# Performance work log

Hardware: AMD Instinct MI355X
Metric: run time of the kernel (lower is better)

## Reference

```python
import jax, jax.numpy as jnp
import numpy as np

B, N, E, F, H, OUT = 128, 2048, 16384, 32, 64, 16


def setup_inputs() -> dict:
    key = jax.random.key(0)
    ks = jax.random.split(key, 8)
    node_features = jax.random.normal(ks[0], (B, N, F), jnp.float32)
    edge_index = jax.random.randint(ks[1], (B, 2, E), 0, N)
    n_nodes = jax.random.randint(ks[2], (B,), N // 2, N + 1)
    # prefix node mask (required for the original's index-consistency)
    node_mask = jnp.arange(N)[None, :] < n_nodes[:, None]
    glorot = lambda k, sh, fan: jax.random.normal(k, sh, jnp.float32) / np.sqrt(fan)
    return dict(
        node_features=node_features, edge_index=edge_index, node_mask=node_mask,
        W1=glorot(ks[3], (F, H), F), b1=jnp.zeros((H,), jnp.float32),
        W2=glorot(ks[4], (H, H), H), b2=jnp.zeros((H,), jnp.float32),
        aW1=glorot(ks[5], (H, H), H), ab1=jnp.zeros((H,), jnp.float32),
        aW2=glorot(ks[6], (H, OUT), H), ab2=jnp.zeros((OUT,), jnp.float32),
    )


def reference(node_features, edge_index, node_mask, W1, b1, W2, b2, aW1, ab1, aW2, ab2):
    x = node_features
    src, dst = edge_index[:, 0], edge_index[:, 1]          # [B,E] source->target
    n = node_mask.sum(-1)                                   # [B] valid nodes per graph
    max_idx = n - 1
    emask = (src <= max_idx[:, None]) & (dst <= max_idx[:, None])
    w = emask.astype(x.dtype)                               # [B,E] edge weights

    # flatten batch into one big segment space [B*N]
    offs = (jnp.arange(B, dtype=src.dtype) * N)[:, None]
    src_f = (src + offs).reshape(-1)
    dst_f = (dst + offs).reshape(-1)
    w_f = w.reshape(-1)

    # GCN normalization with self-loops (PyG GCNConv default)
    deg = jax.ops.segment_sum(w_f, dst_f, num_segments=B * N).reshape(B, N)
    deg = deg + node_mask.astype(x.dtype)                   # self-loop weight 1 on valid nodes
    dis = jnp.where(deg > 0, jax.lax.rsqrt(deg), 0.0)       # deg^{-1/2}, [B,N]
    dis_f = dis.reshape(-1)
    norm = dis_f[src_f] * dis_f[dst_f] * w_f                # [B*E]
    nmask_f = node_mask.reshape(-1).astype(x.dtype)[:, None]
    nmask = node_mask.astype(x.dtype)[..., None]

    def gcn_relu(h, W, bias):
        hW = (h @ W).reshape(B * N, -1)                     # transform first (PyG order)
        msgs = hW[src_f] * norm[:, None]                    # [B*E, H]
        agg = jax.ops.segment_sum(msgs, dst_f, num_segments=B * N)
        agg = agg + hW * ((dis * dis).reshape(-1)[:, None] * nmask_f)  # self-loop term
        out = (agg.reshape(B, N, -1) + bias) * nmask
        return jax.nn.relu(out)

    h1 = gcn_relu(x * nmask, W1, b1)
    h2 = gcn_relu(h1, W2, b2)

    # mean pool over valid nodes (zeros if empty graph)
    pooled = h2.sum(1) / jnp.maximum(n, 1)[:, None].astype(x.dtype)
    hidden = jax.nn.relu(pooled @ aW1 + ab1)
    logits = hidden @ aW2 + ab2                             # [B, OUT]
    return logits
```

## Files before the change

### kernel.cpp

```cpp
#include <hip/hip_runtime.h>
#include <hip/hip_bf16.h>

#define B 128
#define N 2048
#define E 16384
#define F 32
#define H 64
#define OUTD 16
#define CAP 16
#define NP1 (N + 1)

typedef __attribute__((ext_vector_type(8))) short bf16x8;
typedef __attribute__((ext_vector_type(4))) float f32x4;

__device__ __forceinline__ float b2f(unsigned short u) {
    return __uint_as_float(((unsigned int)u) << 16);
}
__device__ __forceinline__ unsigned short f2b(float f) {
    unsigned int x = __float_as_uint(f);
    unsigned int r = (x + 0x7FFFu + ((x >> 16) & 1u)) >> 16;
    return (unsigned short)r;
}
__device__ __forceinline__ unsigned int pack2(float a, float b) {
    return (unsigned int)f2b(a) | ((unsigned int)f2b(b) << 16);
}

__device__ __forceinline__ void add8(float (&a)[8], uint4 u) {
    a[0] += __uint_as_float(u.x << 16);
    a[1] += __uint_as_float(u.x & 0xffff0000u);
    a[2] += __uint_as_float(u.y << 16);
    a[3] += __uint_as_float(u.y & 0xffff0000u);
    a[4] += __uint_as_float(u.z << 16);
    a[5] += __uint_as_float(u.z & 0xffff0000u);
    a[6] += __uint_as_float(u.w << 16);
    a[7] += __uint_as_float(u.w & 0xffff0000u);
}
__device__ __forceinline__ void fma8(float (&a)[8], uint4 u, float w) {
    a[0] = fmaf(__uint_as_float(u.x << 16), w, a[0]);
    a[1] = fmaf(__uint_as_float(u.x & 0xffff0000u), w, a[1]);
    a[2] = fmaf(__uint_as_float(u.y << 16), w, a[2]);
    a[3] = fmaf(__uint_as_float(u.y & 0xffff0000u), w, a[3]);
    a[4] = fmaf(__uint_as_float(u.z << 16), w, a[4]);
    a[5] = fmaf(__uint_as_float(u.z & 0xffff0000u), w, a[5]);
    a[6] = fmaf(__uint_as_float(u.w << 16), w, a[6]);
    a[7] = fmaf(__uint_as_float(u.w & 0xffff0000u), w, a[7]);
}

struct PrepArgs {
    const void* src[9];
    void* dst[9];
};

__global__ __launch_bounds__(1024) void k_build(
    const void* __restrict__ x, const int* __restrict__ eidx,
    const void* __restrict__ mask, PrepArgs pa, int* __restrict__ flags,
    int* __restrict__ n_arr, float* __restrict__ dis,
    unsigned char* __restrict__ degc, unsigned short* __restrict__ ssrc,
    int2* __restrict__ ovf, int* __restrict__ ovf_cnt,
    float* __restrict__ pooled, unsigned int* __restrict__ xconv,
    unsigned int* __restrict__ z_u) {
    __shared__ int s_cnt[N];
    __shared__ float s_fred[16];
    __shared__ int s_w[16];
    __shared__ int s_n, s_ovf, s_xbf, s_pf;
    const int b = blockIdx.x;
    const int t = threadIdx.x;
    const int bN = b * N;
    {
        const unsigned short* p = (const unsigned short*)x;
        float s = fminf(fabsf(b2f(p[t])), 1e6f);
        for (int o = 32; o > 0; o >>= 1) s += __shfl_down(s, o);
        if ((t & 63) == 0) s_fred[t >> 6] = s;
        __syncthreads();
        if (t == 0) {
            float a = 0.f;
            for (int i = 0; i < 16; i++) a += s_fred[i];
            int f = (a < 100.0f * 1024.0f) ? 1 : 0;
            s_xbf = f;
            if (b == 0) flags[0] = f;
        }
    }
    const unsigned char* mb = (const unsigned char*)mask;
    int mode;
    if (mb[0] == 0x80 && mb[1] == 0x3F) mode = 2;
    else if (mb[0] != 0 && mb[1] != 0) mode = 0;
    else if (mb[0] != 0) mode = (mb[4] != 0) ? 1 : 4;
    else mode = 3;
    int cnt = 0;
    if (mode == 0) {
        const unsigned char* r = mb + (size_t)b * N;
        for (int i = t; i < N; i += 1024) cnt += (r[i] != 0);
    } else if (mode == 1 || mode == 3) {
        const unsigned int* r = (const unsigned int*)mask + (size_t)b * N;
        for (int i = t; i < N; i += 1024) cnt += (r[i] != 0);
    } else if (mode == 2) {
        const unsigned short* r = (const unsigned short*)mask + (size_t)b * N;
        for (int i = t; i < N; i += 1024) cnt += (r[i] != 0);
    } else {
        const unsigned long long* r = (const unsigned long long*)mask + (size_t)b * N;
        for (int i = t; i < N; i += 1024) cnt += (r[i] != 0ULL);
    }
    for (int o = 32; o > 0; o >>= 1) cnt += __shfl_down(cnt, o);
    if ((t & 63) == 0) s_w[t >> 6] = cnt;
    for (int i = t; i < N; i += 1024) s_cnt[i] = 0;
    if (t >= 32 && t < 64) z_u[((size_t)b * NP1 + N) * (H / 2) + (t - 32)] = 0u;
    if (t == 0) s_ovf = 0;
    __syncthreads();
    if (t == 0) {
        int a = 0;
        for (int i = 0; i < 16; i++) a += s_w[i];
        s_n = a > N ? N : a;
    }
    __syncthreads();
    const int n = s_n;
    const int4* es4 = (const int4*)(eidx + (size_t)b * 2 * E);
    const int4* ed4 = es4 + E / 4;
    int4 sv[4], dv4[4];
#pragma unroll
    for (int k = 0; k < 4; k++) {
        sv[k] = es4[t + k * 1024];
        dv4[k] = ed4[t + k * 1024];
    }
#pragma unroll
    for (int k = 0; k < 4; k++) {
        int4 s4 = sv[k], d4 = dv4[k];
#define FILL1(SS, DD)                                                          \
        if ((unsigned)(SS) < (unsigned)n && (unsigned)(DD) < (unsigned)n) {    \
            int pos = atomicAdd(&s_cnt[DD], 1);                                \
            if (pos < CAP)                                                     \
                ssrc[((size_t)(bN + (DD))) * CAP + pos] = (unsigned short)(SS);\
            else {                                                             \
                int oi = atomicAdd(&s_ovf, 1);                                 \
                if (oi < E) ovf[(size_t)b * E + oi] = make_int2((DD), (SS));   \
            }                                                                  \
        }
        FILL1(s4.x, d4.x) FILL1(s4.y, d4.y) FILL1(s4.z, d4.z) FILL1(s4.w, d4.w)
#undef FILL1
    }
    __syncthreads();
    for (int v = t; v < N; v += 1024) {
        int c = s_cnt[v];
        dis[bN + v] = (v < n) ? rsqrtf((float)(c + 1)) : 0.0f;
        degc[bN + v] = (unsigned char)(c < CAP ? c : CAP);
    }
    if (t < H) pooled[b * H + t] = 0.0f;
    if (t == 0) { n_arr[b] = n; ovf_cnt[b] = s_ovf; }
    if (!s_xbf) {
        const float4* xp = (const float4*)((const float*)x + (size_t)bN * F);
        uint2* yp = (uint2*)(xconv + (size_t)bN * (F / 2));
        for (int i = t; i < N * F / 4; i += 1024) {
            float4 v4 = xp[i];
            yp[i] = make_uint2(pack2(v4.x, v4.y), pack2(v4.z, v4.w));
        }
    }
    if (b >= 1 && b <= 8) {
        int sz;
        switch (b) {
            case 1: sz = F * H; break;
            case 2: sz = H; break;
            case 3: sz = H * H; break;
            case 4: sz = H; break;
            case 5: sz = H * H; break;
            case 6: sz = H; break;
            case 7: sz = H * OUTD; break;
            default: sz = OUTD; break;
        }
        const int K = sz < 1024 ? sz : 1024;
        const unsigned short* p = (const unsigned short*)pa.src[b];
        float s = (t < K) ? fminf(fabsf(b2f(p[t])), 1e6f) : 0.f;
        for (int o = 32; o > 0; o >>= 1) s += __shfl_down(s, o);
        __syncthreads();
        if ((t & 63) == 0) s_fred[t >> 6] = s;
        __syncthreads();
        if (t == 0) {
            float a = 0.f;
            for (int i = 0; i < 16; i++) a += s_fred[i];
            s_pf = (a < 100.0f * (float)K) ? 1 : 0;
        }
        __syncthreads();
        const int fl = s_pf;
        auto rd = [&](int i) -> float {
            return fl ? b2f(((const unsigned short*)pa.src[b])[i])
                      : ((const float*)pa.src[b])[i];
        };
        if (b == 1) {
            unsigned short* dst = (unsigned short*)pa.dst[b];
            for (int i = t; i < F * H; i += 1024) {
                int k = i >> 6, n2 = i & 63;
                dst[n2 * 40 + k] = f2b(rd(i));
            }
        } else if (b == 3) {
            unsigned short* dst = (unsigned short*)pa.dst[b];
            for (int i = t; i < H * H; i += 1024) {
                int k = i >> 6, n2 = i & 63;
                dst[n2 * 72 + k] = f2b(rd(i));
            }
        } else {
            float* dst = (float*)pa.dst[b];
            for (int i = t; i < sz; i += 1024) dst[i] = rd(i);
        }
    }
}

__global__ __launch_bounds__(256) void k_agg_gemm1(
    const void* __restrict__ x, const unsigned int* __restrict__ xconv,
    const int* __restrict__ flags, const float* __restrict__ dis,
    const unsigned char* __restrict__ degc, const unsigned short* __restrict__ ssrc,
    const int2* __restrict__ ovf, const int* __restrict__ ovf_cnt,
    const unsigned short* __restrict__ w1t, const float* __restrict__ b1f,
    unsigned short* __restrict__ zs) {
    __shared__ unsigned short s_e[64 * CAP];
    __shared__ unsigned char s_dg[64];
    __shared__ float s_dv[64];
    __shared__ float s_b1[64];
    __shared__ __align__(16) unsigned short s_w1t[64 * 40];
    __shared__ __align__(16) unsigned short s_a1[64 * 40];
    const int bid = blockIdx.x;
    const int b = (bid & 7) + ((bid >> 8) << 3);
    const int v0 = ((bid >> 3) & 31) * 64;
    const int t = threadIdx.x;
    const int bN = b * N;
    if (t < 128) ((int4*)s_e)[t] = ((const int4*)(ssrc + (size_t)(bN + v0) * CAP))[t];
    if (t >= 128 && t < 144)
        ((unsigned int*)s_dg)[t - 128] = ((const unsigned int*)(degc + bN + v0))[t - 128];
    if (t >= 192) s_dv[t - 192] = dis[bN + v0 + (t - 192)];
    if (t >= 144 && t < 208) s_b1[t - 144] = b1f[t - 144];
    for (int i = t; i < 320; i += 256) ((int4*)s_w1t)[i] = ((const int4*)w1t)[i];
    __syncthreads();
    const int lane = t & 63;
    const int w = t >> 6;
    const int oc = ovf_cnt[b];
    const unsigned int* yb =
        (flags[0] ? (const unsigned int*)x : xconv) + (size_t)bN * (F / 2);
    const float* disb = dis + bN;
    {
        const int nn = w * 16 + (lane >> 2);
        const int v = v0 + nn;
        const int cu = (lane & 3) * 4;
        const int dg = s_dg[nn];
        const float dv = s_dv[nn];
        int md = s_dg[w * 16 + (lane & 15)];
        int m2;
        m2 = __shfl_xor(md, 1); md = md > m2 ? md : m2;
        m2 = __shfl_xor(md, 2); md = md > m2 ? md : m2;
        m2 = __shfl_xor(md, 4); md = md > m2 ? md : m2;
        m2 = __shfl_xor(md, 8); md = md > m2 ? md : m2;
        const unsigned short* ep = &s_e[nn * CAP];
        float a[8] = {0.f, 0.f, 0.f, 0.f, 0.f, 0.f, 0.f, 0.f};
        uint4 rs = *(const uint4*)(yb + (size_t)v * (F / 2) + cu);
        int i0 = ep[0] & (N - 1);
        int i1 = ep[1] & (N - 1);
        uint4 r0 = *(const uint4*)(yb + (size_t)i0 * (F / 2) + cu);
        float w0p = disb[i0];
        uint4 r1 = *(const uint4*)(yb + (size_t)i1 * (F / 2) + cu);
        float w1p = disb[i1];
        fma8(a, rs, dv);
        for (int s = 0; s < md; s++) {
            int sn = s + 2; sn = sn > CAP - 1 ? CAP - 1 : sn;
            int i2 = ep[sn] & (N - 1);
            uint4 r2 = *(const uint4*)(yb + (size_t)i2 * (F / 2) + cu);
            float w2p = disb[i2];
            fma8(a, r0, s < dg ? w0p : 0.0f);
            r0 = r1; w0p = w1p; r1 = r2; w1p = w2p;
        }
        if (oc > 0) {
            const int2* ob = ovf + (size_t)b * E;
            for (int j = 0; j < oc; j++) {
                int2 o = ob[j];
                if (o.x == v) {
                    uint4 u4 = *(const uint4*)(yb + (size_t)o.y * (F / 2) + cu);
                    fma8(a, u4, disb[o.y]);
                }
            }
        }
        uint4 ovv;
        ovv.x = pack2(a[0] * dv, a[1] * dv);
        ovv.y = pack2(a[2] * dv, a[3] * dv);
        ovv.z = pack2(a[4] * dv, a[5] * dv);
        ovv.w = pack2(a[6] * dv, a[7] * dv);
        *(uint4*)((unsigned int*)s_a1 + nn * 20 + cu) = ovv;
    }
    __syncthreads();
    const int quad = lane >> 4;
    const int f2 = lane & 15;
    const int m0 = w * 16;
    bf16x8 af = *(const bf16x8*)&s_a1[(m0 + f2) * 40 + quad * 8];
    float dvr[4];
#pragma unroll
    for (int r = 0; r < 4; r++) dvr[r] = s_dv[m0 + quad * 4 + r];
#pragma unroll
    for (int nt = 0; nt < 4; nt++) {
        bf16x8 bf = *(const bf16x8*)&s_w1t[(nt * 16 + f2) * 40 + quad * 8];
        f32x4 acc = {0.f, 0.f, 0.f, 0.f};
        acc = __builtin_amdgcn_mfma_f32_16x16x32_bf16(af, bf, acc, 0, 0, 0);
        float bb = s_b1[nt * 16 + f2];
#pragma unroll
        for (int r = 0; r < 4; r++) {
            int row = m0 + quad * 4 + r;
            float val = dvr[r] * fmaxf(acc[r] + bb, 0.0f);
            zs[((size_t)b * NP1 + v0 + row) * H + nt * 16 + f2] = f2b(val);
        }
    }
}

__global__ __launch_bounds__(256) void k_agg_gemm2_pool(
    const unsigned int* __restrict__ z_u, const float* __restrict__ dis,
    const unsigned char* __restrict__ degc, const unsigned short* __restrict__ ssrc,
    const int2* __restrict__ ovf, const int* __restrict__ ovf_cnt,
    const unsigned short* __restrict__ w2t, const float* __restrict__ b2f_,
    float* __restrict__ pooled) {
    __shared__ unsigned short s_e[64 * CAP];
    __shared__ unsigned char s_dg[64];
    __shared__ float s_dv[64];
    __shared__ float s_b2[64];
    __shared__ __align__(16) unsigned short s_w2t[64 * 72];
    __shared__ __align__(16) unsigned short s_a2[64 * 72];
    __shared__ float s_pool[4][64];
    const int bid = blockIdx.x;
    const int b = (bid & 7) + ((bid >> 8) << 3);
    const int v0 = ((bid >> 3) & 31) * 64;
    const int t = threadIdx.x;
    const int bN = b * N;
    if (t < 128) ((int4*)s_e)[t] = ((const int4*)(ssrc + (size_t)(bN + v0) * CAP))[t];
    if (t >= 128 && t < 144)
        ((unsigned int*)s_dg)[t - 128] = ((const unsigned int*)(degc + bN + v0))[t - 128];
    if (t >= 192) s_dv[t - 192] = dis[bN + v0 + (t - 192)];
    if (t >= 144 && t < 208) s_b2[t - 144] = b2f_[t - 144];
    for (int i = t; i < 576; i += 256) ((int4*)s_w2t)[i] = ((const int4*)w2t)[i];
    __syncthreads();
    const int lane = t & 63;
    const int w = t >> 6;
    const int oc = ovf_cnt[b];
    const unsigned int* zb = z_u + (size_t)b * NP1 * (H / 2);
#pragma unroll
    for (int g = 0; g < 2; g++) {
        const int nn = w * 16 + g * 8 + (lane >> 3);
        const int v = v0 + nn;
        const int cu = (lane & 7) * 4;
        const int dg = s_dg[nn];
        int md = s_dg[w * 16 + g * 8 + (lane & 7)];
        int m2;
        m2 = __shfl_xor(md, 1); md = md > m2 ? md : m2;
        m2 = __shfl_xor(md, 2); md = md > m2 ? md : m2;
        m2 = __shfl_xor(md, 4); md = md > m2 ? md : m2;
        const unsigned short* ep = &s_e[nn * CAP];
        float a[8] = {0.f, 0.f, 0.f, 0.f, 0.f, 0.f, 0.f, 0.f};
        uint4 cur = *(const uint4*)(zb + (size_t)v * (H / 2) + cu);
        int i0 = (0 < dg) ? (ep[0] & (N - 1)) : N;
        uint4 nxt = *(const uint4*)(zb + (size_t)i0 * (H / 2) + cu);
        for (int s = 0; s < md; s++) {
            int sn = s + 1; sn = sn > CAP - 1 ? CAP - 1 : sn;
            int i2 = (s + 1 < dg) ? (ep[sn] & (N - 1)) : N;
            uint4 n2 = *(const uint4*)(zb + (size_t)i2 * (H / 2) + cu);
            add8(a, cur);
            cur = nxt; nxt = n2;
        }
        add8(a, cur);
        if (oc > 0) {
            const int2* ob = ovf + (size_t)b * E;
            for (int j = 0; j < oc; j++) {
                int2 o = ob[j];
                if (o.x == v) {
                    uint4 u4 = *(const uint4*)(zb + (size_t)o.y * (H / 2) + cu);
                    add8(a, u4);
                }
            }
        }
        const float dv = s_dv[nn];
        uint4 ovv;
        ovv.x = pack2(a[0] * dv, a[1] * dv);
        ovv.y = pack2(a[2] * dv, a[3] * dv);
        ovv.z = pack2(a[4] * dv, a[5] * dv);
        ovv.w = pack2(a[6] * dv, a[7] * dv);
        *(uint4*)((unsigned int*)s_a2 + nn * 36 + cu) = ovv;
    }
    __syncthreads();
    const int quad = lane >> 4;
    const int f2 = lane & 15;
    const int m0 = w * 16;
    bf16x8 af0 = *(const bf16x8*)&s_a2[(m0 + f2) * 72 + quad * 8];
    bf16x8 af1 = *(const bf16x8*)&s_a2[(m0 + f2) * 72 + 32 + quad * 8];
    float dvr[4];
#pragma unroll
    for (int r = 0; r < 4; r++) dvr[r] = s_dv[m0 + quad * 4 + r];
#pragma unroll
    for (int nt = 0; nt < 4; nt++) {
        bf16x8 bf0 = *(const bf16x8*)&s_w2t[(nt * 16 + f2) * 72 + quad * 8];
        bf16x8 bf1 = *(const bf16x8*)&s_w2t[(nt * 16 + f2) * 72 + 32 + quad * 8];
        f32x4 acc = {0.f, 0.f, 0.f, 0.f};
        acc = __builtin_amdgcn_mfma_f32_16x16x32_bf16(af0, bf0, acc, 0, 0, 0);
        acc = __builtin_amdgcn_mfma_f32_16x16x32_bf16(af1, bf1, acc, 0, 0, 0);
        float bb = s_b2[nt * 16 + f2];
        float ps = 0.f;
#pragma unroll
        for (int r = 0; r < 4; r++)
            ps += (dvr[r] > 0.0f) ? fmaxf(acc[r] + bb, 0.0f) : 0.0f;
        ps += __shfl_xor(ps, 16);
        ps += __shfl_xor(ps, 32);
        if (quad == 0) s_pool[w][nt * 16 + f2] = ps;
    }
    __syncthreads();
    if (t < H)
        atomicAdd(&pooled[b * H + t],
                  s_pool[0][t] + s_pool[1][t] + s_pool[2][t] + s_pool[3][t]);
}

__global__ __launch_bounds__(64) void k_mlp(
    const float* __restrict__ pooled, const int* __restrict__ n_arr,
    const float* __restrict__ aW1, const float* __restrict__ ab1,
    const float* __restrict__ aW2, const float* __restrict__ ab2,
    const int* __restrict__ flags, void* __restrict__ out) {
    const int b = blockIdx.x;
    const int t = threadIdx.x;
    __shared__ float p[64];
    __shared__ float hid[64];
    int n = n_arr[b];
    if (n < 1) n = 1;
    p[t] = pooled[b * H + t] / (float)n;
    __syncthreads();
    float acc = ab1[t];
    for (int j = 0; j < 64; j++) acc += p[j] * aW1[j * 64 + t];
    hid[t] = fmaxf(acc, 0.0f);
    __syncthreads();
    if (t < 16) {
        float a2 = ab2[t];
        for (int j = 0; j < 64; j++) a2 += hid[j] * aW2[j * 16 + t];
        if (flags[0]) ((unsigned short*)out)[b * OUTD + t] = f2b(a2);
        else          ((float*)out)[b * OUTD + t] = a2;
    }
}

extern "C" void kernel_launch(void* const* d_in, const int* in_sizes, int n_in,
                              void* d_out, int out_size, void* d_ws, size_t ws_size,
                              hipStream_t stream) {
    const void* x    = d_in[0];
    const int*  eidx = (const int*)d_in[1];
    const void* mask = d_in[2];

    char* ws = (char*)d_ws;
    size_t off = 0;
    auto alloc = [&](size_t bytes) -> void* {
        void* p = ws + off;
        off += (bytes + 255) & ~(size_t)255;
        return p;
    };
    int*   flags   = (int*)alloc(16 * sizeof(int));
    unsigned short* w1t = (unsigned short*)alloc(64 * 40 * 2);
    unsigned short* w2t = (unsigned short*)alloc(64 * 72 * 2);
    float* b1f     = (float*)alloc(H * sizeof(float));
    float* b2f_    = (float*)alloc(H * sizeof(float));
    float* aW1f    = (float*)alloc(H * H * sizeof(float));
    float* ab1f    = (float*)alloc(H * sizeof(float));
    float* aW2f    = (float*)alloc(H * OUTD * sizeof(float));
    float* ab2f    = (float*)alloc(OUTD * sizeof(float));
    int*   n_arr   = (int*)alloc(B * sizeof(int));
    float* dis     = (float*)alloc((size_t)B * N * sizeof(float));
    unsigned char*  degc = (unsigned char*)alloc((size_t)B * N);
    unsigned short* ssrc = (unsigned short*)alloc((size_t)B * N * CAP * 2);
    int2*  ovf     = (int2*)alloc((size_t)B * E * sizeof(int2));
    int*   ovf_cnt = (int*)alloc(B * sizeof(int));
    float* pooled  = (float*)alloc((size_t)B * H * sizeof(float));
    unsigned int* xconv = (unsigned int*)alloc((size_t)B * N * (F / 2) * 4);
    unsigned int* z_u = (unsigned int*)alloc((size_t)B * NP1 * (H / 2) * 4);

    PrepArgs pa;
    pa.src[0] = x;        pa.dst[0] = pooled;
    pa.src[1] = d_in[3];  pa.dst[1] = w1t;
    pa.src[2] = d_in[4];  pa.dst[2] = b1f;
    pa.src[3] = d_in[5];  pa.dst[3] = w2t;
    pa.src[4] = d_in[6];  pa.dst[4] = b2f_;
    pa.src[5] = d_in[7];  pa.dst[5] = aW1f;
    pa.src[6] = d_in[8];  pa.dst[6] = ab1f;
    pa.src[7] = d_in[9];  pa.dst[7] = aW2f;
    pa.src[8] = d_in[10]; pa.dst[8] = ab2f;

    k_build<<<B, 1024, 0, stream>>>(x, eidx, mask, pa, flags, n_arr, dis, degc,
                                    ssrc, ovf, ovf_cnt, pooled, xconv, z_u);
    k_agg_gemm1<<<B * 32, 256, 0, stream>>>(x, xconv, flags, dis, degc, ssrc,
                                            ovf, ovf_cnt, w1t, b1f,
                                            (unsigned short*)z_u);
    k_agg_gemm2_pool<<<B * 32, 256, 0, stream>>>(z_u, dis, degc, ssrc, ovf,
                                                 ovf_cnt, w2t, b2f_, pooled);
    k_mlp<<<B, 64, 0, stream>>>(pooled, n_arr, aW1f, ab1f, aW2f, ab2f, flags, d_out);
}
```

Measured before the change: 165.6 us.

## Sort nodes by in-degree so aggregation warps see uniform loop trip counts

```diff
diff --git a/kernel.cpp b/kernel.cpp
--- a/kernel.cpp
+++ b/kernel.cpp
@@ -25,16 +25,6 @@
     return (unsigned int)f2b(a) | ((unsigned int)f2b(b) << 16);
 }
 
-__device__ __forceinline__ void add8(float (&a)[8], uint4 u) {
-    a[0] += __uint_as_float(u.x << 16);
-    a[1] += __uint_as_float(u.x & 0xffff0000u);
-    a[2] += __uint_as_float(u.y << 16);
-    a[3] += __uint_as_float(u.y & 0xffff0000u);
-    a[4] += __uint_as_float(u.z << 16);
-    a[5] += __uint_as_float(u.z & 0xffff0000u);
-    a[6] += __uint_as_float(u.w << 16);
-    a[7] += __uint_as_float(u.w & 0xffff0000u);
-}
 __device__ __forceinline__ void fma8(float (&a)[8], uint4 u, float w) {
     a[0] = fmaf(__uint_as_float(u.x << 16), w, a[0]);
     a[1] = fmaf(__uint_as_float(u.x & 0xffff0000u), w, a[1]);
@@ -58,10 +48,11 @@
     unsigned char* __restrict__ degc, unsigned short* __restrict__ ssrc,
     int2* __restrict__ ovf, int* __restrict__ ovf_cnt,
     float* __restrict__ pooled, unsigned int* __restrict__ xconv,
-    unsigned int* __restrict__ z_u) {
+    unsigned short* __restrict__ permg) {
     __shared__ int s_cnt[N];
     __shared__ float s_fred[16];
     __shared__ int s_w[16];
+    __shared__ int s_hist[CAP + 1];
     __shared__ int s_n, s_ovf, s_xbf, s_pf;
     const int b = blockIdx.x;
     const int t = threadIdx.x;
@@ -103,7 +94,7 @@
     for (int o = 32; o > 0; o >>= 1) cnt += __shfl_down(cnt, o);
     if ((t & 63) == 0) s_w[t >> 6] = cnt;
     for (int i = t; i < N; i += 1024) s_cnt[i] = 0;
-    if (t >= 32 && t < 64) z_u[((size_t)b * NP1 + N) * (H / 2) + (t - 32)] = 0u;
+    if (t <= CAP) s_hist[t] = 0;
     if (t == 0) s_ovf = 0;
     __syncthreads();
     if (t == 0) {
@@ -142,9 +133,21 @@
         int c = s_cnt[v];
         dis[bN + v] = (v < n) ? rsqrtf((float)(c + 1)) : 0.0f;
         degc[bN + v] = (unsigned char)(c < CAP ? c : CAP);
+        atomicAdd(&s_hist[c < CAP ? c : CAP], 1);
     }
     if (t < H) pooled[b * H + t] = 0.0f;
     if (t == 0) { n_arr[b] = n; ovf_cnt[b] = s_ovf; }
+    __syncthreads();
+    if (t == 0) {
+        int run = 0;
+        for (int i = 0; i <= CAP; i++) { int h = s_hist[i]; s_hist[i] = run; run += h; }
+    }
+    __syncthreads();
+    for (int v = t; v < N; v += 1024) {
+        int c = s_cnt[v];
+        int pos = atomicAdd(&s_hist[c < CAP ? c : CAP], 1);
+        permg[bN + pos] = (unsigned short)v;
+    }
     if (!s_xbf) {
         const float4* xp = (const float4*)((const float*)x + (size_t)bN * F);
         uint2* yp = (uint2*)(xconv + (size_t)bN * (F / 2));
@@ -206,13 +209,15 @@
     const void* __restrict__ x, const unsigned int* __restrict__ xconv,
     const int* __restrict__ flags, const float* __restrict__ dis,
     const unsigned char* __restrict__ degc, const unsigned short* __restrict__ ssrc,
+    const unsigned short* __restrict__ permg,
     const int2* __restrict__ ovf, const int* __restrict__ ovf_cnt,
     const unsigned short* __restrict__ w1t, const float* __restrict__ b1f,
     unsigned short* __restrict__ zs) {
-    __shared__ unsigned short s_e[64 * CAP];
+    __shared__ __align__(16) unsigned short s_vp[64];
+    __shared__ __align__(16) unsigned short s_e[64 * CAP];
     __shared__ unsigned char s_dg[64];
-    __shared__ float s_dv[64];
     __shared__ float s_b1[64];
+    __shared__ __align__(16) float s_dis[N];
     __shared__ __align__(16) unsigned short s_w1t[64 * 40];
     __shared__ __align__(16) unsigned short s_a1[64 * 40];
     const int bid = blockIdx.x;
@@ -220,25 +225,30 @@
     const int v0 = ((bid >> 3) & 31) * 64;
     const int t = threadIdx.x;
     const int bN = b * N;
-    if (t < 128) ((int4*)s_e)[t] = ((const int4*)(ssrc + (size_t)(bN + v0) * CAP))[t];
-    if (t >= 128 && t < 144)
-        ((unsigned int*)s_dg)[t - 128] = ((const unsigned int*)(degc + bN + v0))[t - 128];
-    if (t >= 192) s_dv[t - 192] = dis[bN + v0 + (t - 192)];
+    if (t < 8) ((int4*)s_vp)[t] = ((const int4*)(permg + bN + v0))[t];
     if (t >= 144 && t < 208) s_b1[t - 144] = b1f[t - 144];
     for (int i = t; i < 320; i += 256) ((int4*)s_w1t)[i] = ((const int4*)w1t)[i];
+    for (int i = t; i < 512; i += 256)
+        ((float4*)s_dis)[i] = ((const float4*)(dis + bN))[i];
+    __syncthreads();
+    if (t < 128) {
+        int vp = s_vp[t >> 1];
+        ((int4*)s_e)[t] = ((const int4*)(ssrc + (size_t)(bN + vp) * CAP))[t & 1];
+    } else if (t < 192) {
+        s_dg[t - 128] = degc[bN + s_vp[t - 128]];
+    }
     __syncthreads();
     const int lane = t & 63;
     const int w = t >> 6;
     const int oc = ovf_cnt[b];
     const unsigned int* yb =
         (flags[0] ? (const unsigned int*)x : xconv) + (size_t)bN * (F / 2);
-    const float* disb = dis + bN;
     {
         const int nn = w * 16 + (lane >> 2);
-        const int v = v0 + nn;
+        const int vp = s_vp[nn];
         const int cu = (lane & 3) * 4;
         const int dg = s_dg[nn];
-        const float dv = s_dv[nn];
+        const float dv = s_dis[vp];
         int md = s_dg[w * 16 + (lane & 15)];
         int m2;
         m2 = __shfl_xor(md, 1); md = md > m2 ? md : m2;
@@ -247,29 +257,29 @@
         m2 = __shfl_xor(md, 8); md = md > m2 ? md : m2;
         const unsigned short* ep = &s_e[nn * CAP];
         float a[8] = {0.f, 0.f, 0.f, 0.f, 0.f, 0.f, 0.f, 0.f};
-        uint4 rs = *(const uint4*)(yb + (size_t)v * (F / 2) + cu);
+        uint4 rs = *(const uint4*)(yb + (size_t)vp * (F / 2) + cu);
+        fma8(a, rs, dv);
         int i0 = ep[0] & (N - 1);
         int i1 = ep[1] & (N - 1);
         uint4 r0 = *(const uint4*)(yb + (size_t)i0 * (F / 2) + cu);
-        float w0p = disb[i0];
+        float w0p = (0 < dg) ? s_dis[i0] : 0.f;
         uint4 r1 = *(const uint4*)(yb + (size_t)i1 * (F / 2) + cu);
-        float w1p = disb[i1];
-        fma8(a, rs, dv);
+        float w1p = (1 < dg) ? s_dis[i1] : 0.f;
         for (int s = 0; s < md; s++) {
             int sn = s + 2; sn = sn > CAP - 1 ? CAP - 1 : sn;
             int i2 = ep[sn] & (N - 1);
             uint4 r2 = *(const uint4*)(yb + (size_t)i2 * (F / 2) + cu);
-            float w2p = disb[i2];
-            fma8(a, r0, s < dg ? w0p : 0.0f);
+            float w2p = (s + 2 < dg) ? s_dis[i2] : 0.f;
+            fma8(a, r0, w0p);
             r0 = r1; w0p = w1p; r1 = r2; w1p = w2p;
         }
         if (oc > 0) {
             const int2* ob = ovf + (size_t)b * E;
             for (int j = 0; j < oc; j++) {
                 int2 o = ob[j];
-                if (o.x == v) {
+                if (o.x == vp) {
                     uint4 u4 = *(const uint4*)(yb + (size_t)o.y * (F / 2) + cu);
-                    fma8(a, u4, disb[o.y]);
+                    fma8(a, u4, s_dis[o.y]);
                 }
             }
         }
@@ -286,8 +296,12 @@
     const int m0 = w * 16;
     bf16x8 af = *(const bf16x8*)&s_a1[(m0 + f2) * 40 + quad * 8];
     float dvr[4];
-#pragma unroll
-    for (int r = 0; r < 4; r++) dvr[r] = s_dv[m0 + quad * 4 + r];
+    int vpr[4];
+#pragma unroll
+    for (int r = 0; r < 4; r++) {
+        vpr[r] = s_vp[m0 + quad * 4 + r];
+        dvr[r] = s_dis[vpr[r]];
+    }
 #pragma unroll
     for (int nt = 0; nt < 4; nt++) {
         bf16x8 bf = *(const bf16x8*)&s_w1t[(nt * 16 + f2) * 40 + quad * 8];
@@ -296,9 +310,8 @@
         float bb = s_b1[nt * 16 + f2];
 #pragma unroll
         for (int r = 0; r < 4; r++) {
-            int row = m0 + quad * 4 + r;
             float val = dvr[r] * fmaxf(acc[r] + bb, 0.0f);
-            zs[((size_t)b * NP1 + v0 + row) * H + nt * 16 + f2] = f2b(val);
+            zs[((size_t)b * NP1 + vpr[r]) * H + nt * 16 + f2] = f2b(val);
         }
     }
 }
@@ -306,10 +319,12 @@
 __global__ __launch_bounds__(256) void k_agg_gemm2_pool(
     const unsigned int* __restrict__ z_u, const float* __restrict__ dis,
     const unsigned char* __restrict__ degc, const unsigned short* __restrict__ ssrc,
+    const unsigned short* __restrict__ permg,
     const int2* __restrict__ ovf, const int* __restrict__ ovf_cnt,
     const unsigned short* __restrict__ w2t, const float* __restrict__ b2f_,
     float* __restrict__ pooled) {
-    __shared__ unsigned short s_e[64 * CAP];
+    __shared__ __align__(16) unsigned short s_vp[64];
+    __shared__ __align__(16) unsigned short s_e[64 * CAP];
     __shared__ unsigned char s_dg[64];
     __shared__ float s_dv[64];
     __shared__ float s_b2[64];
@@ -321,12 +336,18 @@
     const int v0 = ((bid >> 3) & 31) * 64;
     const int t = threadIdx.x;
     const int bN = b * N;
-    if (t < 128) ((int4*)s_e)[t] = ((const int4*)(ssrc + (size_t)(bN + v0) * CAP))[t];
-    if (t >= 128 && t < 144)
-        ((unsigned int*)s_dg)[t - 128] = ((const unsigned int*)(degc + bN + v0))[t - 128];
-    if (t >= 192) s_dv[t - 192] = dis[bN + v0 + (t - 192)];
+    if (t < 8) ((int4*)s_vp)[t] = ((const int4*)(permg + bN + v0))[t];
     if (t >= 144 && t < 208) s_b2[t - 144] = b2f_[t - 144];
     for (int i = t; i < 576; i += 256) ((int4*)s_w2t)[i] = ((const int4*)w2t)[i];
+    __syncthreads();
+    if (t < 128) {
+        int vp = s_vp[t >> 1];
+        ((int4*)s_e)[t] = ((const int4*)(ssrc + (size_t)(bN + vp) * CAP))[t & 1];
+    } else if (t < 192) {
+        s_dg[t - 128] = degc[bN + s_vp[t - 128]];
+    } else {
+        s_dv[t - 192] = dis[bN + s_vp[t - 192]];
+    }
     __syncthreads();
     const int lane = t & 63;
     const int w = t >> 6;
@@ -335,7 +356,7 @@
 #pragma unroll
     for (int g = 0; g < 2; g++) {
         const int nn = w * 16 + g * 8 + (lane >> 3);
-        const int v = v0 + nn;
+        const int vp = s_vp[nn];
         const int cu = (lane & 7) * 4;
         const int dg = s_dg[nn];
         int md = s_dg[w * 16 + g * 8 + (lane & 7)];
@@ -345,24 +366,29 @@
         m2 = __shfl_xor(md, 4); md = md > m2 ? md : m2;
         const unsigned short* ep = &s_e[nn * CAP];
         float a[8] = {0.f, 0.f, 0.f, 0.f, 0.f, 0.f, 0.f, 0.f};
-        uint4 cur = *(const uint4*)(zb + (size_t)v * (H / 2) + cu);
-        int i0 = (0 < dg) ? (ep[0] & (N - 1)) : N;
-        uint4 nxt = *(const uint4*)(zb + (size_t)i0 * (H / 2) + cu);
+        uint4 rs = *(const uint4*)(zb + (size_t)vp * (H / 2) + cu);
+        fma8(a, rs, 1.0f);
+        int i0 = ep[0] & (N - 1);
+        int i1 = ep[1] & (N - 1);
+        uint4 r0 = *(const uint4*)(zb + (size_t)i0 * (H / 2) + cu);
+        float w0p = (0 < dg) ? 1.0f : 0.f;
+        uint4 r1 = *(const uint4*)(zb + (size_t)i1 * (H / 2) + cu);
+        float w1p = (1 < dg) ? 1.0f : 0.f;
         for (int s = 0; s < md; s++) {
-            int sn = s + 1; sn = sn > CAP - 1 ? CAP - 1 : sn;
-            int i2 = (s + 1 < dg) ? (ep[sn] & (N - 1)) : N;
-            uint4 n2 = *(const uint4*)(zb + (size_t)i2 * (H / 2) + cu);
-            add8(a, cur);
-            cur = nxt; nxt = n2;
-        }
-        add8(a, cur);
+            int sn = s + 2; sn = sn > CAP - 1 ? CAP - 1 : sn;
+            int i2 = ep[sn] & (N - 1);
+            uint4 r2 = *(const uint4*)(zb + (size_t)i2 * (H / 2) + cu);
+            float w2p = (s + 2 < dg) ? 1.0f : 0.f;
+            fma8(a, r0, w0p);
+            r0 = r1; w0p = w1p; r1 = r2; w1p = w2p;
+        }
         if (oc > 0) {
             const int2* ob = ovf + (size_t)b * E;
             for (int j = 0; j < oc; j++) {
                 int2 o = ob[j];
-                if (o.x == v) {
+                if (o.x == vp) {
                     uint4 u4 = *(const uint4*)(zb + (size_t)o.y * (H / 2) + cu);
-                    add8(a, u4);
+                    fma8(a, u4, 1.0f);
                 }
             }
         }
@@ -457,6 +483,7 @@
     float* dis     = (float*)alloc((size_t)B * N * sizeof(float));
     unsigned char*  degc = (unsigned char*)alloc((size_t)B * N);
     unsigned short* ssrc = (unsigned short*)alloc((size_t)B * N * CAP * 2);
+    unsigned short* permg = (unsigned short*)alloc((size_t)B * N * 2);
     int2*  ovf     = (int2*)alloc((size_t)B * E * sizeof(int2));
     int*   ovf_cnt = (int*)alloc(B * sizeof(int));
     float* pooled  = (float*)alloc((size_t)B * H * sizeof(float));
@@ -475,11 +502,12 @@
     pa.src[8] = d_in[10]; pa.dst[8] = ab2f;
 
     k_build<<<B, 1024, 0, stream>>>(x, eidx, mask, pa, flags, n_arr, dis, degc,
-                                    ssrc, ovf, ovf_cnt, pooled, xconv, z_u);
+                                    ssrc, ovf, ovf_cnt, pooled, xconv, permg);
     k_agg_gemm1<<<B * 32, 256, 0, stream>>>(x, xconv, flags, dis, degc, ssrc,
-                                            ovf, ovf_cnt, w1t, b1f,
+                                            permg, ovf, ovf_cnt, w1t, b1f,
                                             (unsigned short*)z_u);
-    k_agg_gemm2_pool<<<B * 32, 256, 0, stream>>>(z_u, dis, degc, ssrc, ovf,
-                                                 ovf_cnt, w2t, b2f_, pooled);
+    k_agg_gemm2_pool<<<B * 32, 256, 0, stream>>>(z_u, dis, degc, ssrc, permg,
+                                                 ovf, ovf_cnt, w2t, b2f_,
+                                                 pooled);
     k_mlp<<<B, 64, 0, stream>>>(pooled, n_arr, aW1f, ab1f, aW2f, ab2f, flags, d_out);
 }
```

After: 164.6 us. About the same (-0.6%).

## Split graph build into prep and 4-way-parallel CSR kernels with global atomics

Applied to the files above, without the earlier changes.

```diff
diff --git a/kernel.cpp b/kernel.cpp
--- a/kernel.cpp
+++ b/kernel.cpp
@@ -25,6 +25,16 @@
     return (unsigned int)f2b(a) | ((unsigned int)f2b(b) << 16);
 }
 
+__device__ __forceinline__ void fma8(float (&a)[8], uint4 u, float w) {
+    a[0] = fmaf(__uint_as_float(u.x << 16), w, a[0]);
+    a[1] = fmaf(__uint_as_float(u.x & 0xffff0000u), w, a[1]);
+    a[2] = fmaf(__uint_as_float(u.y << 16), w, a[2]);
+    a[3] = fmaf(__uint_as_float(u.y & 0xffff0000u), w, a[3]);
+    a[4] = fmaf(__uint_as_float(u.z << 16), w, a[4]);
+    a[5] = fmaf(__uint_as_float(u.z & 0xffff0000u), w, a[5]);
+    a[6] = fmaf(__uint_as_float(u.w << 16), w, a[6]);
+    a[7] = fmaf(__uint_as_float(u.w & 0xffff0000u), w, a[7]);
+}
 __device__ __forceinline__ void add8(float (&a)[8], uint4 u) {
     a[0] += __uint_as_float(u.x << 16);
     a[1] += __uint_as_float(u.x & 0xffff0000u);
@@ -35,46 +45,33 @@
     a[6] += __uint_as_float(u.w << 16);
     a[7] += __uint_as_float(u.w & 0xffff0000u);
 }
-__device__ __forceinline__ void fma8(float (&a)[8], uint4 u, float w) {
-    a[0] = fmaf(__uint_as_float(u.x << 16), w, a[0]);
-    a[1] = fmaf(__uint_as_float(u.x & 0xffff0000u), w, a[1]);
-    a[2] = fmaf(__uint_as_float(u.y << 16), w, a[2]);
-    a[3] = fmaf(__uint_as_float(u.y & 0xffff0000u), w, a[3]);
-    a[4] = fmaf(__uint_as_float(u.z << 16), w, a[4]);
-    a[5] = fmaf(__uint_as_float(u.z & 0xffff0000u), w, a[5]);
-    a[6] = fmaf(__uint_as_float(u.w << 16), w, a[6]);
-    a[7] = fmaf(__uint_as_float(u.w & 0xffff0000u), w, a[7]);
-}
 
 struct PrepArgs {
     const void* src[9];
     void* dst[9];
 };
 
-__global__ __launch_bounds__(1024) void k_build(
-    const void* __restrict__ x, const int* __restrict__ eidx,
-    const void* __restrict__ mask, PrepArgs pa, int* __restrict__ flags,
-    int* __restrict__ n_arr, float* __restrict__ dis,
-    unsigned char* __restrict__ degc, unsigned short* __restrict__ ssrc,
-    int2* __restrict__ ovf, int* __restrict__ ovf_cnt,
-    float* __restrict__ pooled, unsigned int* __restrict__ xconv,
-    unsigned int* __restrict__ z_u) {
-    __shared__ int s_cnt[N];
-    __shared__ float s_fred[16];
-    __shared__ int s_w[16];
-    __shared__ int s_n, s_ovf, s_xbf, s_pf;
+__global__ __launch_bounds__(256) void k_pre(
+    const void* __restrict__ x, const void* __restrict__ mask, PrepArgs pa,
+    int* __restrict__ flags, int* __restrict__ n_arr, int* __restrict__ deg,
+    int* __restrict__ ovf_cnt, float* __restrict__ pooled,
+    unsigned int* __restrict__ xconv, unsigned int* __restrict__ z_u) {
+    __shared__ float s_fred[4];
+    __shared__ int s_w[4];
+    __shared__ int s_n, s_xbf, s_pf;
     const int b = blockIdx.x;
     const int t = threadIdx.x;
     const int bN = b * N;
     {
         const unsigned short* p = (const unsigned short*)x;
-        float s = fminf(fabsf(b2f(p[t])), 1e6f);
+        float s = 0.f;
+#pragma unroll
+        for (int k = 0; k < 4; k++) s += fminf(fabsf(b2f(p[t + k * 256])), 1e6f);
         for (int o = 32; o > 0; o >>= 1) s += __shfl_down(s, o);
         if ((t & 63) == 0) s_fred[t >> 6] = s;
         __syncthreads();
         if (t == 0) {
-            float a = 0.f;
-            for (int i = 0; i < 16; i++) a += s_fred[i];
+            float a = s_fred[0] + s_fred[1] + s_fred[2] + s_fred[3];
             int f = (a < 100.0f * 1024.0f) ? 1 : 0;
             s_xbf = f;
             if (b == 0) flags[0] = f;
@@ -89,66 +86,39 @@
     int cnt = 0;
     if (mode == 0) {
         const unsigned char* r = mb + (size_t)b * N;
-        for (int i = t; i < N; i += 1024) cnt += (r[i] != 0);
+        for (int i = t; i < N; i += 256) cnt += (r[i] != 0);
     } else if (mode == 1 || mode == 3) {
         const unsigned int* r = (const unsigned int*)mask + (size_t)b * N;
-        for (int i = t; i < N; i += 1024) cnt += (r[i] != 0);
+        for (int i = t; i < N; i += 256) cnt += (r[i] != 0);
     } else if (mode == 2) {
         const unsigned short* r = (const unsigned short*)mask + (size_t)b * N;
-        for (int i = t; i < N; i += 1024) cnt += (r[i] != 0);
+        for (int i = t; i < N; i += 256) cnt += (r[i] != 0);
     } else {
         const unsigned long long* r = (const unsigned long long*)mask + (size_t)b * N;
-        for (int i = t; i < N; i += 1024) cnt += (r[i] != 0ULL);
+        for (int i = t; i < N; i += 256) cnt += (r[i] != 0ULL);
     }
     for (int o = 32; o > 0; o >>= 1) cnt += __shfl_down(cnt, o);
     if ((t & 63) == 0) s_w[t >> 6] = cnt;
-    for (int i = t; i < N; i += 1024) s_cnt[i] = 0;
-    if (t >= 32 && t < 64) z_u[((size_t)b * NP1 + N) * (H / 2) + (t - 32)] = 0u;
-    if (t == 0) s_ovf = 0;
     __syncthreads();
     if (t == 0) {
-        int a = 0;
-        for (int i = 0; i < 16; i++) a += s_w[i];
+        int a = s_w[0] + s_w[1] + s_w[2] + s_w[3];
         s_n = a > N ? N : a;
-    }
-    __syncthreads();
-    const int n = s_n;
-    const int4* es4 = (const int4*)(eidx + (size_t)b * 2 * E);
-    const int4* ed4 = es4 + E / 4;
-    int4 sv[4], dv4[4];
-#pragma unroll
-    for (int k = 0; k < 4; k++) {
-        sv[k] = es4[t + k * 1024];
-        dv4[k] = ed4[t + k * 1024];
-    }
-#pragma unroll
-    for (int k = 0; k < 4; k++) {
-        int4 s4 = sv[k], d4 = dv4[k];
-#define FILL1(SS, DD)                                                          \
-        if ((unsigned)(SS) < (unsigned)n && (unsigned)(DD) < (unsigned)n) {    \
-            int pos = atomicAdd(&s_cnt[DD], 1);                                \
-            if (pos < CAP)                                                     \
-                ssrc[((size_t)(bN + (DD))) * CAP + pos] = (unsigned short)(SS);\
-            else {                                                             \
-                int oi = atomicAdd(&s_ovf, 1);                                 \
-                if (oi < E) ovf[(size_t)b * E + oi] = make_int2((DD), (SS));   \
-            }                                                                  \
-        }
-        FILL1(s4.x, d4.x) FILL1(s4.y, d4.y) FILL1(s4.z, d4.z) FILL1(s4.w, d4.w)
-#undef FILL1
-    }
-    __syncthreads();
-    for (int v = t; v < N; v += 1024) {
-        int c = s_cnt[v];
-        dis[bN + v] = (v < n) ? rsqrtf((float)(c + 1)) : 0.0f;
-        degc[bN + v] = (unsigned char)(c < CAP ? c : CAP);
+        n_arr[b] = s_n;
+        ovf_cnt[b] = 0;
+    }
+    {
+        int4* dp = (int4*)(deg + bN);
+        const int4 zz = make_int4(0, 0, 0, 0);
+        dp[t] = zz;
+        dp[t + 256] = zz;
     }
     if (t < H) pooled[b * H + t] = 0.0f;
-    if (t == 0) { n_arr[b] = n; ovf_cnt[b] = s_ovf; }
+    if (t >= 64 && t < 96) z_u[((size_t)b * NP1 + N) * (H / 2) + (t - 64)] = 0u;
+    __syncthreads();
     if (!s_xbf) {
         const float4* xp = (const float4*)((const float*)x + (size_t)bN * F);
         uint2* yp = (uint2*)(xconv + (size_t)bN * (F / 2));
-        for (int i = t; i < N * F / 4; i += 1024) {
+        for (int i = t; i < N * F / 4; i += 256) {
             float4 v4 = xp[i];
             yp[i] = make_uint2(pack2(v4.x, v4.y), pack2(v4.z, v4.w));
         }
@@ -167,14 +137,14 @@
         }
         const int K = sz < 1024 ? sz : 1024;
         const unsigned short* p = (const unsigned short*)pa.src[b];
-        float s = (t < K) ? fminf(fabsf(b2f(p[t])), 1e6f) : 0.f;
+        float s = 0.f;
+        for (int i = t; i < K; i += 256) s += fminf(fabsf(b2f(p[i])), 1e6f);
         for (int o = 32; o > 0; o >>= 1) s += __shfl_down(s, o);
         __syncthreads();
         if ((t & 63) == 0) s_fred[t >> 6] = s;
         __syncthreads();
         if (t == 0) {
-            float a = 0.f;
-            for (int i = 0; i < 16; i++) a += s_fred[i];
+            float a = s_fred[0] + s_fred[1] + s_fred[2] + s_fred[3];
             s_pf = (a < 100.0f * (float)K) ? 1 : 0;
         }
         __syncthreads();
@@ -185,34 +155,70 @@
         };
         if (b == 1) {
             unsigned short* dst = (unsigned short*)pa.dst[b];
-            for (int i = t; i < F * H; i += 1024) {
+            for (int i = t; i < F * H; i += 256) {
                 int k = i >> 6, n2 = i & 63;
                 dst[n2 * 40 + k] = f2b(rd(i));
             }
         } else if (b == 3) {
             unsigned short* dst = (unsigned short*)pa.dst[b];
-            for (int i = t; i < H * H; i += 1024) {
+            for (int i = t; i < H * H; i += 256) {
                 int k = i >> 6, n2 = i & 63;
                 dst[n2 * 72 + k] = f2b(rd(i));
             }
         } else {
             float* dst = (float*)pa.dst[b];
-            for (int i = t; i < sz; i += 1024) dst[i] = rd(i);
-        }
+            for (int i = t; i < sz; i += 256) dst[i] = rd(i);
+        }
+    }
+}
+
+__global__ __launch_bounds__(256) void k_csr(
+    const int* __restrict__ eidx, const int* __restrict__ n_arr,
+    int* __restrict__ deg, unsigned short* __restrict__ ssrc,
+    int2* __restrict__ ovf, int* __restrict__ ovf_cnt) {
+    const int q = blockIdx.x;
+    const int b = q >> 2;
+    const int quarter = q & 3;
+    const int t = threadIdx.x;
+    const int bN = b * N;
+    const int n = n_arr[b];
+    const int4* es4 = (const int4*)(eidx + (size_t)b * 2 * E) + quarter * 1024;
+    const int4* ed4 = es4 + E / 4;
+    int4 sv[4], dv4[4];
+#pragma unroll
+    for (int k = 0; k < 4; k++) {
+        sv[k] = es4[t + k * 256];
+        dv4[k] = ed4[t + k * 256];
+    }
+#pragma unroll
+    for (int k = 0; k < 4; k++) {
+        int4 s4 = sv[k], d4 = dv4[k];
+#define FILL1(SS, DD)                                                          \
+        if ((unsigned)(SS) < (unsigned)n && (unsigned)(DD) < (unsigned)n) {    \
+            int pos = atomicAdd(&deg[bN + (DD)], 1);                           \
+            if (pos < CAP)                                                     \
+                ssrc[((size_t)(bN + (DD))) * CAP + pos] = (unsigned short)(SS);\
+            else {                                                             \
+                int oi = atomicAdd(&ovf_cnt[b], 1);                            \
+                if (oi < E) ovf[(size_t)b * E + oi] = make_int2((DD), (SS));   \
+            }                                                                  \
+        }
+        FILL1(s4.x, d4.x) FILL1(s4.y, d4.y) FILL1(s4.z, d4.z) FILL1(s4.w, d4.w)
+#undef FILL1
     }
 }
 
 __global__ __launch_bounds__(256) void k_agg_gemm1(
     const void* __restrict__ x, const unsigned int* __restrict__ xconv,
-    const int* __restrict__ flags, const float* __restrict__ dis,
-    const unsigned char* __restrict__ degc, const unsigned short* __restrict__ ssrc,
+    const int* __restrict__ flags, const int* __restrict__ deg,
+    const int* __restrict__ n_arr, const unsigned short* __restrict__ ssrc,
     const int2* __restrict__ ovf, const int* __restrict__ ovf_cnt,
     const unsigned short* __restrict__ w1t, const float* __restrict__ b1f,
     unsigned short* __restrict__ zs) {
-    __shared__ unsigned short s_e[64 * CAP];
+    __shared__ __align__(16) unsigned short s_e[64 * CAP];
     __shared__ unsigned char s_dg[64];
-    __shared__ float s_dv[64];
     __shared__ float s_b1[64];
+    __shared__ __align__(16) float s_dis[N];
     __shared__ __align__(16) unsigned short s_w1t[64 * 40];
     __shared__ __align__(16) unsigned short s_a1[64 * 40];
     const int bid = blockIdx.x;
@@ -220,25 +226,31 @@
     const int v0 = ((bid >> 3) & 31) * 64;
     const int t = threadIdx.x;
     const int bN = b * N;
+    const int n = n_arr[b];
     if (t < 128) ((int4*)s_e)[t] = ((const int4*)(ssrc + (size_t)(bN + v0) * CAP))[t];
-    if (t >= 128 && t < 144)
-        ((unsigned int*)s_dg)[t - 128] = ((const unsigned int*)(degc + bN + v0))[t - 128];
-    if (t >= 192) s_dv[t - 192] = dis[bN + v0 + (t - 192)];
-    if (t >= 144 && t < 208) s_b1[t - 144] = b1f[t - 144];
+    if (t >= 128 && t < 192) {
+        int c = deg[bN + v0 + (t - 128)];
+        s_dg[t - 128] = (unsigned char)(c < CAP ? c : CAP);
+    }
+    if (t >= 192) s_b1[t - 192] = b1f[t - 192];
+    if (t < 64) s_b1[t] = b1f[t];
     for (int i = t; i < 320; i += 256) ((int4*)s_w1t)[i] = ((const int4*)w1t)[i];
+    for (int i = t; i < N; i += 256) {
+        int c = deg[bN + i];
+        s_dis[i] = (i < n) ? rsqrtf((float)(c + 1)) : 0.0f;
+    }
     __syncthreads();
     const int lane = t & 63;
     const int w = t >> 6;
     const int oc = ovf_cnt[b];
     const unsigned int* yb =
         (flags[0] ? (const unsigned int*)x : xconv) + (size_t)bN * (F / 2);
-    const float* disb = dis + bN;
     {
         const int nn = w * 16 + (lane >> 2);
         const int v = v0 + nn;
         const int cu = (lane & 3) * 4;
         const int dg = s_dg[nn];
-        const float dv = s_dv[nn];
+        const float dv = s_dis[v];
         int md = s_dg[w * 16 + (lane & 15)];
         int m2;
         m2 = __shfl_xor(md, 1); md = md > m2 ? md : m2;
@@ -248,19 +260,19 @@
         const unsigned short* ep = &s_e[nn * CAP];
         float a[8] = {0.f, 0.f, 0.f, 0.f, 0.f, 0.f, 0.f, 0.f};
         uint4 rs = *(const uint4*)(yb + (size_t)v * (F / 2) + cu);
+        fma8(a, rs, dv);
         int i0 = ep[0] & (N - 1);
         int i1 = ep[1] & (N - 1);
         uint4 r0 = *(const uint4*)(yb + (size_t)i0 * (F / 2) + cu);
-        float w0p = disb[i0];
+        float w0p = (0 < dg) ? s_dis[i0] : 0.f;
         uint4 r1 = *(const uint4*)(yb + (size_t)i1 * (F / 2) + cu);
-        float w1p = disb[i1];
-        fma8(a, rs, dv);
+        float w1p = (1 < dg) ? s_dis[i1] : 0.f;
         for (int s = 0; s < md; s++) {
             int sn = s + 2; sn = sn > CAP - 1 ? CAP - 1 : sn;
             int i2 = ep[sn] & (N - 1);
             uint4 r2 = *(const uint4*)(yb + (size_t)i2 * (F / 2) + cu);
-            float w2p = disb[i2];
-            fma8(a, r0, s < dg ? w0p : 0.0f);
+            float w2p = (s + 2 < dg) ? s_dis[i2] : 0.f;
+            fma8(a, r0, w0p);
             r0 = r1; w0p = w1p; r1 = r2; w1p = w2p;
         }
         if (oc > 0) {
@@ -269,7 +281,7 @@
                 int2 o = ob[j];
                 if (o.x == v) {
                     uint4 u4 = *(const uint4*)(yb + (size_t)o.y * (F / 2) + cu);
-                    fma8(a, u4, disb[o.y]);
+                    fma8(a, u4, s_dis[o.y]);
                 }
             }
         }
@@ -287,7 +299,7 @@
     bf16x8 af = *(const bf16x8*)&s_a1[(m0 + f2) * 40 + quad * 8];
     float dvr[4];
 #pragma unroll
-    for (int r = 0; r < 4; r++) dvr[r] = s_dv[m0 + quad * 4 + r];
+    for (int r = 0; r < 4; r++) dvr[r] = s_dis[v0 + m0 + quad * 4 + r];
 #pragma unroll
     for (int nt = 0; nt < 4; nt++) {
         bf16x8 bf = *(const bf16x8*)&s_w1t[(nt * 16 + f2) * 40 + quad * 8];
@@ -304,12 +316,12 @@
 }
 
 __global__ __launch_bounds__(256) void k_agg_gemm2_pool(
-    const unsigned int* __restrict__ z_u, const float* __restrict__ dis,
-    const unsigned char* __restrict__ degc, const unsigned short* __restrict__ ssrc,
+    const unsigned int* __restrict__ z_u, const int* __restrict__ deg,
+    const int* __restrict__ n_arr, const unsigned short* __restrict__ ssrc,
     const int2* __restrict__ ovf, const int* __restrict__ ovf_cnt,
     const unsigned short* __restrict__ w2t, const float* __restrict__ b2f_,
     float* __restrict__ pooled) {
-    __shared__ unsigned short s_e[64 * CAP];
+    __shared__ __align__(16) unsigned short s_e[64 * CAP];
     __shared__ unsigned char s_dg[64];
     __shared__ float s_dv[64];
     __shared__ float s_b2[64];
@@ -321,10 +333,17 @@
     const int v0 = ((bid >> 3) & 31) * 64;
     const int t = threadIdx.x;
     const int bN = b * N;
+    const int n = n_arr[b];
     if (t < 128) ((int4*)s_e)[t] = ((const int4*)(ssrc + (size_t)(bN + v0) * CAP))[t];
-    if (t >= 128 && t < 144)
-        ((unsigned int*)s_dg)[t - 128] = ((const unsigned int*)(degc + bN + v0))[t - 128];
-    if (t >= 192) s_dv[t - 192] = dis[bN + v0 + (t - 192)];
+    if (t >= 128 && t < 192) {
+        int c = deg[bN + v0 + (t - 128)];
+        s_dg[t - 128] = (unsigned char)(c < CAP ? c : CAP);
+    }
+    if (t >= 192) {
+        int v = v0 + (t - 192);
+        int c = deg[bN + v];
+        s_dv[t - 192] = (v < n) ? rsqrtf((float)(c + 1)) : 0.0f;
+    }
     if (t >= 144 && t < 208) s_b2[t - 144] = b2f_[t - 144];
     for (int i = t; i < 576; i += 256) ((int4*)s_w2t)[i] = ((const int4*)w2t)[i];
     __syncthreads();
@@ -454,8 +473,7 @@
     float* aW2f    = (float*)alloc(H * OUTD * sizeof(float));
     float* ab2f    = (float*)alloc(OUTD * sizeof(float));
     int*   n_arr   = (int*)alloc(B * sizeof(int));
-    float* dis     = (float*)alloc((size_t)B * N * sizeof(float));
-    unsigned char*  degc = (unsigned char*)alloc((size_t)B * N);
+    int*   deg     = (int*)alloc((size_t)B * N * sizeof(int));
     unsigned short* ssrc = (unsigned short*)alloc((size_t)B * N * CAP * 2);
     int2*  ovf     = (int2*)alloc((size_t)B * E * sizeof(int2));
     int*   ovf_cnt = (int*)alloc(B * sizeof(int));
@@ -474,12 +492,13 @@
     pa.src[7] = d_in[9];  pa.dst[7] = aW2f;
     pa.src[8] = d_in[10]; pa.dst[8] = ab2f;
 
-    k_build<<<B, 1024, 0, stream>>>(x, eidx, mask, pa, flags, n_arr, dis, degc,
-                                    ssrc, ovf, ovf_cnt, pooled, xconv, z_u);
-    k_agg_gemm1<<<B * 32, 256, 0, stream>>>(x, xconv, flags, dis, degc, ssrc,
+    k_pre<<<B, 256, 0, stream>>>(x, mask, pa, flags, n_arr, deg, ovf_cnt,
+                                 pooled, xconv, z_u);
+    k_csr<<<B * 4, 256, 0, stream>>>(eidx, n_arr, deg, ssrc, ovf, ovf_cnt);
+    k_agg_gemm1<<<B * 32, 256, 0, stream>>>(x, xconv, flags, deg, n_arr, ssrc,
                                             ovf, ovf_cnt, w1t, b1f,
                                             (unsigned short*)z_u);
-    k_agg_gemm2_pool<<<B * 32, 256, 0, stream>>>(z_u, dis, degc, ssrc, ovf,
+    k_agg_gemm2_pool<<<B * 32, 256, 0, stream>>>(z_u, deg, n_arr, ssrc, ovf,
                                                  ovf_cnt, w2t, b2f_, pooled);
     k_mlp<<<B, 64, 0, stream>>>(pooled, n_arr, aW1f, ab1f, aW2f, ab2f, flags, d_out);
 }
```

After: 489.6 us. 2.96x slower.
